# Kernel optimization log

Hardware: AMD Instinct MI355X
Metric: run time of the kernel (lower is better)

Reference implementation:

```python
import jax, jax.numpy as jnp
import numpy as np

DIM = 256
HALF = DIM // 2
B, S = 32, 4096
U_MAX = 4096          # upper bound on number of unique tree positions (positions < S)
MAX_DEPTH = 13        # bitlen(S) covers all path lengths for positions <= S


def setup_inputs() -> dict:
    key = jax.random.key(0)
    k1, k2, k3, k4, k5 = jax.random.split(key, 5)
    token_types = jax.random.randint(k1, (B, S), 0, 5, dtype=jnp.int32)
    node_positions = jax.random.randint(k2, (B, S), 0, S, dtype=jnp.int32)
    small_vals = jax.random.randint(k3, (B, S), 0, 4, dtype=jnp.int32)
    # deBruijn tokens (type 4) reference tree positions -> values must lie in unique(node_positions)
    token_values = jnp.where(token_types == 4, node_positions,
                   jnp.where(token_types == 3, -1, small_vals)).astype(jnp.int32)
    primitives = jax.random.normal(k4, (2, HALF, HALF), dtype=jnp.float32)
    identity = jnp.ones((1, HALF), dtype=jnp.float32)
    embed_weight = jax.random.normal(k5, (11, HALF), dtype=jnp.float32)
    return {"token_types": token_types, "token_values": token_values,
            "node_positions": node_positions, "primitives": primitives,
            "identity": identity, "embed_weight": embed_weight}


def cayley(X):
    # torch orthogonal(..., orthogonal_map='cayley'): A = tril(X) - tril(X)^T (skew), Q = (I - A/2)^{-1}(I + A/2)
    A = jnp.tril(X)
    A = A - jnp.swapaxes(A, -1, -2)
    I = jnp.eye(X.shape[-1], dtype=X.dtype)
    return jnp.linalg.solve(I - 0.5 * A, I + 0.5 * A)


def _forward(token_types, token_values, node_positions, primitives, identity, embed_weight):
    Q = cayley(primitives)                                   # [2, h, h] orthogonal maps
    flat_pos = node_positions.ravel()
    uniq, inv = jnp.unique(flat_pos, return_inverse=True, size=U_MAX, fill_value=S)
    inv = inv.ravel()

    # binary path of pos: bit d of pos for d < bitlen(pos)-1, padded with 2 (pos<=1 -> empty path)
    d = jnp.arange(MAX_DEPTH, dtype=uniq.dtype)
    bits = (uniq[:, None] >> d) & 1                           # [U, D]
    valid = (uniq[:, None] >> (d + 1)) > 0
    word = jnp.where(valid, bits, 2)                          # [U, D]

    maps0 = jnp.broadcast_to(identity, (U_MAX, HALF)).astype(primitives.dtype)

    def step(maps, b):                                        # maps [U, h], b [U]
        m0 = maps @ Q[0].T                                    # linear(maps, primitives[0])
        m1 = maps @ Q[1].T
        maps = jnp.where((b == 0)[:, None], m0,
                jnp.where((b == 1)[:, None], m1, maps))
        return maps, None

    path_emb, _ = jax.lax.scan(step, maps0, word.T)           # [U, h]

    pos_enc = path_emb[inv].reshape(B, S, HALF)               # positional encodings

    sos = token_types == 0
    bop = token_types == 1
    nop = token_types == 2
    oos = (token_types == 3) & (token_values == -1)
    db = token_types == 4

    emb_idx = jnp.where(bop, token_values + 1,
              jnp.where(nop, token_values + 5, 0))
    type_emb = embed_weight[emb_idx]                          # [B, S, h]

    db_idx = jnp.searchsorted(uniq, jnp.clip(token_values, 0, S - 1))  # bucketize into unique positions
    db_emb = path_emb[db_idx]                                 # [B, S, h]

    content = jnp.zeros_like(pos_enc)
    content = jnp.where(sos[..., None], embed_weight[0], content)
    content = jnp.where((bop | nop)[..., None], type_emb, content)
    content = jnp.where(db[..., None], db_emb, content)
    content = jnp.where(oos[..., None], embed_weight[10], content)

    return jnp.concatenate([content, pos_enc], axis=-1)       # [B, S, DIM]


def reference(token_types, token_values, node_positions, primitives, identity, embed_weight):
    return _forward(token_types, token_values, node_positions, primitives, identity, embed_weight)
```

## Files before the change

### kernel.cpp

```cpp
#include <hip/hip_runtime.h>

#define HALF 128
#define NMAT 16384
#define NTOK 131072

typedef float f4 __attribute__((ext_vector_type(4)));

__global__ __launch_bounds__(512) void cayley_qt(const float* __restrict__ prim,
                                                 float* __restrict__ QT) {
    __shared__ __align__(16) float Xs[128 * 129];
    __shared__ __align__(16) float CpT[2][16][132];
    __shared__ __align__(16) float Rp [2][16][128];
    __shared__ __align__(16) float Dcol[2][16][20];

    const int b = blockIdx.x;
    const float* __restrict__ X = prim + b * NMAT;
    const int t  = threadIdx.x;
    const int c  = t & 127;
    const int q  = t >> 7;
    const int r0 = q << 5;

    for (int idx4 = t; idx4 < 4096; idx4 += 512) {
        int gi = idx4 << 2;
        float4 v = *(const float4*)(X + gi);
        int r = gi >> 7, cc = gi & 127;
        float* p = &Xs[r * 129 + cc];
        p[0] = v.x; p[1] = v.y; p[2] = v.z; p[3] = v.w;
    }
    __syncthreads();

    float reg[32];
    #pragma unroll
    for (int i = 0; i < 32; ++i) {
        int r  = r0 + i;
        int mx = r > c ? r : c;
        int mn = r ^ c ^ mx;
        float x = Xs[mx * 129 + mn];
        reg[i] = (r == c) ? 1.0f : (r > c ? 0.5f * x : -0.5f * x);
    }

    #pragma unroll
    for (int s = 0; s < 8; ++s) {
        const int  p     = s & 1;
        const int  k0    = s << 4;
        const int  q0    = s >> 1;
        const int  kl    = (s & 1) << 4;
        const bool panel = (c >= k0) && (c < k0 + 16);

        if (panel) {
            const int m = c - k0;
            #pragma unroll
            for (int i = 0; i < 32; i += 4)
                *(float4*)&CpT[p][m][r0 + i] =
                    make_float4(reg[i], reg[i+1], reg[i+2], reg[i+3]);
        }
        if (q == q0) {
            #pragma unroll
            for (int j = 0; j < 16; ++j) Rp[p][j][c] = reg[kl + j];
        }
        __syncthreads();

        if (t < 64) {
            const int cp = t & 15, q4 = t >> 4;
            float dd[4];
            #pragma unroll
            for (int i = 0; i < 4; ++i) dd[i] = Rp[p][q4 * 4 + i][k0 + cp];
            #pragma unroll
            for (int k = 0; k < 16; ++k) {
                float cv[4];
                #pragma unroll
                for (int i = 0; i < 4; ++i) cv[i] = __shfl(dd[i], (q4 << 4) | k);
                float rv   = __shfl(dd[k & 3], ((k >> 2) << 4) | cp);
                float dkk  = __shfl(rv, k);
                float dinv = 1.0f / dkk;
                float sv   = rv * dinv;
                bool  own  = (cp == k);
                float rf   = own ? dinv : sv;
                #pragma unroll
                for (int i = 0; i < 4; ++i)
                    dd[i] = own ? (-dd[i] * dinv) : fmaf(-cv[i], sv, dd[i]);
                dd[k & 3] = (q4 == (k >> 2)) ? rf : dd[k & 3];
            }
            #pragma unroll
            for (int i = 0; i < 4; ++i) Dcol[p][cp][q4 * 4 + i] = dd[i];
        }
        __syncthreads();

        float coeff[16];
        if (!panel) {
            #pragma unroll
            for (int j = 0; j < 16; ++j) coeff[j] = 0.0f;
            #pragma unroll
            for (int j = 0; j < 16; ++j) {
                float rpj = Rp[p][j][c];
                #pragma unroll
                for (int mq = 0; mq < 16; mq += 4) {
                    float4 dv = *(const float4*)&Dcol[p][j][mq];
                    coeff[mq+0] = fmaf(dv.x, rpj, coeff[mq+0]);
                    coeff[mq+1] = fmaf(dv.y, rpj, coeff[mq+1]);
                    coeff[mq+2] = fmaf(dv.z, rpj, coeff[mq+2]);
                    coeff[mq+3] = fmaf(dv.w, rpj, coeff[mq+3]);
                }
            }
        } else {
            const int mp = c - k0;
            #pragma unroll
            for (int j = 0; j < 16; ++j) coeff[j] = Dcol[p][mp][j];
            #pragma unroll
            for (int i = 0; i < 32; ++i) reg[i] = 0.0f;
        }

        #pragma unroll
        for (int m = 0; m < 16; ++m) {
            float cm = coeff[m];
            #pragma unroll
            for (int i = 0; i < 32; i += 4) {
                float4 c4 = *(const float4*)&CpT[p][m][r0 + i];
                reg[i+0] = fmaf(-c4.x, cm, reg[i+0]);
                reg[i+1] = fmaf(-c4.y, cm, reg[i+1]);
                reg[i+2] = fmaf(-c4.z, cm, reg[i+2]);
                reg[i+3] = fmaf(-c4.w, cm, reg[i+3]);
            }
        }
        if (q == q0) {
            #pragma unroll
            for (int j = 0; j < 16; ++j) reg[kl + j] = coeff[j];
        }
    }

    float* __restrict__ out = QT + b * NMAT;
    #pragma unroll
    for (int i = 0; i < 32; ++i) {
        int r = r0 + i;
        out[r * HALF + c] = 2.0f * reg[i] - (r == c ? 1.0f : 0.0f);
    }
}

__global__ __launch_bounds__(256) void path_base(const float* __restrict__ QT,
                                                 const float* __restrict__ ident,
                                                 float* __restrict__ P) {
    __shared__ __align__(16) float vs[2][4][HALF];
    const int t    = threadIdx.x;
    const int rg   = t >> 6;
    const int jj   = (t & 63) << 1;
    const int v    = (blockIdx.x << 2) + rg;
    const int vmax = (blockIdx.x << 2) + 3;

    float2 cv = *(const float2*)&ident[jj];
    *(float2*)&vs[0][rg][jj] = cv;
    __syncthreads();

    int cur = 0;
    for (int d = 0; d < 8; ++d) {
        if ((vmax >> (d + 1)) == 0) break;
        const bool valid = (v >> (d + 1)) > 0;
        const float* __restrict__ Qm = QT + (((v >> d) & 1) ? NMAT : 0);
        float2 acc = make_float2(0.f, 0.f);
        #pragma unroll 4
        for (int cc = 0; cc < 128; cc += 4) {
            float4 v4 = *(const float4*)&vs[cur][rg][cc];
            float2 q0 = *(const float2*)&Qm[(cc+0)*HALF + jj];
            float2 q1 = *(const float2*)&Qm[(cc+1)*HALF + jj];
            float2 q2 = *(const float2*)&Qm[(cc+2)*HALF + jj];
            float2 q3 = *(const float2*)&Qm[(cc+3)*HALF + jj];
            acc.x = fmaf(v4.x,q0.x, fmaf(v4.y,q1.x, fmaf(v4.z,q2.x, fmaf(v4.w,q3.x, acc.x))));
            acc.y = fmaf(v4.x,q0.y, fmaf(v4.y,q1.y, fmaf(v4.z,q2.y, fmaf(v4.w,q3.y, acc.y))));
        }
        if (valid) cv = acc;
        *(float2*)&vs[cur ^ 1][rg][jj] = cv;
        __syncthreads();
        cur ^= 1;
    }
    *(float2*)&P[v * HALF + jj] = cv;
}

__global__ __launch_bounds__(256) void path_upper(const float* __restrict__ QT,
                                                  float* __restrict__ P) {
    __shared__ __align__(16) float vs[2][8][HALF];
    const int t  = threadIdx.x;
    const int j  = t & 127;
    const int h  = t >> 7;
    const int k  = 2 + (blockIdx.x >> 4);
    const int r0 = (blockIdx.x & 15) << 3;

    float acc[4];
    #pragma unroll
    for (int rr = 0; rr < 4; ++rr)
        acc[rr] = P[(128 + r0 + h * 4 + rr) * HALF + j];

    int p = 0;
    for (int d = 7; d < 13; ++d) {
        if ((k >> (d - 6)) == 0) break;
        const float* __restrict__ Qm = QT + (((k >> (d - 7)) & 1) ? NMAT : 0);
        #pragma unroll
        for (int rr = 0; rr < 4; ++rr) vs[p][h * 4 + rr][j] = acc[rr];
        __syncthreads();

        float nacc[4] = {0.f, 0.f, 0.f, 0.f};
        #pragma unroll 4
        for (int cc = 0; cc < 128; cc += 4) {
            float q0 = Qm[(cc + 0) * HALF + j];
            float q1 = Qm[(cc + 1) * HALF + j];
            float q2 = Qm[(cc + 2) * HALF + j];
            float q3 = Qm[(cc + 3) * HALF + j];
            #pragma unroll
            for (int rr = 0; rr < 4; ++rr) {
                float4 v4 = *(const float4*)&vs[p][h * 4 + rr][cc];
                nacc[rr] = fmaf(v4.x, q0,
                           fmaf(v4.y, q1,
                           fmaf(v4.z, q2,
                           fmaf(v4.w, q3, nacc[rr]))));
            }
        }
        #pragma unroll
        for (int rr = 0; rr < 4; ++rr) acc[rr] = nacc[rr];
        p ^= 1;
    }

    #pragma unroll
    for (int rr = 0; rr < 4; ++rr)
        P[((k << 7) | (r0 + h * 4 + rr)) * HALF + j] = acc[rr];
}

__global__ __launch_bounds__(256) void emit_out(const int* __restrict__ tt,
                                                const int* __restrict__ tv,
                                                const int* __restrict__ np,
                                                const float* __restrict__ P,
                                                const float* __restrict__ emb,
                                                float* __restrict__ out) {
    const int i  = (blockIdx.x << 2) + (threadIdx.x >> 6);
    const int jj = (threadIdx.x & 63) << 2;
    const int ty = tt[i];
    const int v  = tv[i];
    f4 val;
    if (jj < 128) {
        if (ty == 0)      val = *(const f4*)&emb[jj];
        else if (ty == 1) val = *(const f4*)&emb[(v + 1) * HALF + jj];
        else if (ty == 2) val = *(const f4*)&emb[(v + 5) * HALF + jj];
        else if (ty == 4) {
            int vc = v < 0 ? 0 : (v > 4095 ? 4095 : v);
            val = *(const f4*)&P[vc * HALF + jj];
        } else if (v == -1) val = *(const f4*)&emb[10 * HALF + jj];
        else { f4 z = {0.f, 0.f, 0.f, 0.f}; val = z; }
    } else {
        const int p = np[i];
        val = *(const f4*)&P[p * HALF + (jj - 128)];
    }
    __builtin_nontemporal_store(val, (f4*)&out[i * 256 + jj]);
}

extern "C" void kernel_launch(void* const* d_in, const int* in_sizes, int n_in,
                              void* d_out, int out_size, void* d_ws, size_t ws_size,
                              hipStream_t stream) {
    const int*   token_types = (const int*)  d_in[0];
    const int*   token_vals  = (const int*)  d_in[1];
    const int*   node_pos    = (const int*)  d_in[2];
    const float* prim        = (const float*)d_in[3];
    const float* ident       = (const float*)d_in[4];
    const float* emb         = (const float*)d_in[5];
    float* out = (float*)d_out;

    float* QT = (float*)d_ws;
    float* P  = (float*)((char*)d_ws + 262144);

    cayley_qt  <<<2,   512, 0, stream>>>(prim, QT);
    path_base  <<<64,  256, 0, stream>>>(QT, ident, P);
    path_upper <<<480, 256, 0, stream>>>(QT, P);
    emit_out   <<<NTOK / 4, 256, 0, stream>>>(token_types, token_vals, node_pos,
                                              P, emb, out);
}
```

Measured before the change: 275.7 us.

## Retile Cayley solve to 4x8 register blocks with precomputed panel update in shared memory

Each thread in the Cayley matrix inversion kernel now holds a 4x8 sub-block instead of a 32-row column strip. Each panel step precomputes the update matrix RB = D*R cooperatively in shared memory, rather than every thread computing its own 16 coefficients redundantly. The rank-16 update then reads row-panel coefficients and RB rows as float4 vectors, and the final stores are vectorized. This cuts redundant FLOPs and improves shared-memory reuse, at the cost of one extra __syncthreads per panel step.

```diff
diff --git a/kernel.cpp b/kernel.cpp
--- a/kernel.cpp
+++ b/kernel.cpp
@@ -9,54 +9,66 @@
 __global__ __launch_bounds__(512) void cayley_qt(const float* __restrict__ prim,
                                                  float* __restrict__ QT) {
     __shared__ __align__(16) float Xs[128 * 129];
-    __shared__ __align__(16) float CpT[2][16][132];
-    __shared__ __align__(16) float Rp [2][16][128];
-    __shared__ __align__(16) float Dcol[2][16][20];
+    __shared__ __align__(16) float Cp[2][128][20];
+    __shared__ __align__(16) float Rp[16][132];
+    __shared__ __align__(16) float Dcol[16][20];
+    __shared__ __align__(16) float RB[16][132];
 
     const int b = blockIdx.x;
     const float* __restrict__ X = prim + b * NMAT;
     const int t  = threadIdx.x;
-    const int c  = t & 127;
-    const int q  = t >> 7;
-    const int r0 = q << 5;
+    const int rg = t >> 4;
+    const int cg = t & 15;
 
     for (int idx4 = t; idx4 < 4096; idx4 += 512) {
         int gi = idx4 << 2;
         float4 v = *(const float4*)(X + gi);
         int r = gi >> 7, cc = gi & 127;
-        float* p = &Xs[r * 129 + cc];
-        p[0] = v.x; p[1] = v.y; p[2] = v.z; p[3] = v.w;
+        float* xp = &Xs[r * 129 + cc];
+        xp[0] = v.x; xp[1] = v.y; xp[2] = v.z; xp[3] = v.w;
     }
     __syncthreads();
 
-    float reg[32];
-    #pragma unroll
-    for (int i = 0; i < 32; ++i) {
-        int r  = r0 + i;
-        int mx = r > c ? r : c;
-        int mn = r ^ c ^ mx;
-        float x = Xs[mx * 129 + mn];
-        reg[i] = (r == c) ? 1.0f : (r > c ? 0.5f * x : -0.5f * x);
+    float reg[4][8];
+    #pragma unroll
+    for (int i = 0; i < 4; ++i) {
+        const int r = (rg << 2) + i;
+        #pragma unroll
+        for (int jj = 0; jj < 8; ++jj) {
+            const int c = (cg << 3) + jj;
+            int mx = r > c ? r : c;
+            int mn = r ^ c ^ mx;
+            float x = Xs[mx * 129 + mn];
+            reg[i][jj] = (r == c) ? 1.0f : (r > c ? 0.5f * x : -0.5f * x);
+        }
     }
 
     #pragma unroll
     for (int s = 0; s < 8; ++s) {
-        const int  p     = s & 1;
-        const int  k0    = s << 4;
-        const int  q0    = s >> 1;
-        const int  kl    = (s & 1) << 4;
-        const bool panel = (c >= k0) && (c < k0 + 16);
-
-        if (panel) {
-            const int m = c - k0;
-            #pragma unroll
-            for (int i = 0; i < 32; i += 4)
-                *(float4*)&CpT[p][m][r0 + i] =
-                    make_float4(reg[i], reg[i+1], reg[i+2], reg[i+3]);
-        }
-        if (q == q0) {
-            #pragma unroll
-            for (int j = 0; j < 16; ++j) Rp[p][j][c] = reg[kl + j];
+        const int  p    = s & 1;
+        const int  k0   = s << 4;
+        const bool pubC = (cg >> 1) == s;
+        const bool pubR = (rg >> 2) == s;
+
+        if (pubC) {
+            const int mb = (cg & 1) << 3;
+            #pragma unroll
+            for (int i = 0; i < 4; ++i) {
+                *(float4*)&Cp[p][(rg << 2) + i][mb] =
+                    make_float4(reg[i][0], reg[i][1], reg[i][2], reg[i][3]);
+                *(float4*)&Cp[p][(rg << 2) + i][mb + 4] =
+                    make_float4(reg[i][4], reg[i][5], reg[i][6], reg[i][7]);
+            }
+        }
+        if (pubR) {
+            const int jb = (rg & 3) << 2;
+            #pragma unroll
+            for (int i = 0; i < 4; ++i) {
+                *(float4*)&Rp[jb + i][cg << 3] =
+                    make_float4(reg[i][0], reg[i][1], reg[i][2], reg[i][3]);
+                *(float4*)&Rp[jb + i][(cg << 3) + 4] =
+                    make_float4(reg[i][4], reg[i][5], reg[i][6], reg[i][7]);
+            }
         }
         __syncthreads();
 
@@ -64,7 +76,7 @@
             const int cp = t & 15, q4 = t >> 4;
             float dd[4];
             #pragma unroll
-            for (int i = 0; i < 4; ++i) dd[i] = Rp[p][q4 * 4 + i][k0 + cp];
+            for (int i = 0; i < 4; ++i) dd[i] = Rp[q4 * 4 + i][k0 + cp];
             #pragma unroll
             for (int k = 0; k < 16; ++k) {
                 float cv[4];
@@ -82,57 +94,96 @@
                 dd[k & 3] = (q4 == (k >> 2)) ? rf : dd[k & 3];
             }
             #pragma unroll
-            for (int i = 0; i < 4; ++i) Dcol[p][cp][q4 * 4 + i] = dd[i];
-        }
-        __syncthreads();
-
-        float coeff[16];
-        if (!panel) {
-            #pragma unroll
-            for (int j = 0; j < 16; ++j) coeff[j] = 0.0f;
-            #pragma unroll
-            for (int j = 0; j < 16; ++j) {
-                float rpj = Rp[p][j][c];
+            for (int i = 0; i < 4; ++i) Dcol[cp][q4 * 4 + i] = dd[i];
+        }
+        __syncthreads();
+
+        {
+            const int m  = t >> 5;
+            const int qd = t & 31;
+            const int cb = qd << 2;
+            float4 acc;
+            if ((qd >> 2) == s) {
+                acc.x = Dcol[cb + 0 - k0][m];
+                acc.y = Dcol[cb + 1 - k0][m];
+                acc.z = Dcol[cb + 2 - k0][m];
+                acc.w = Dcol[cb + 3 - k0][m];
+            } else {
+                acc = make_float4(0.f, 0.f, 0.f, 0.f);
                 #pragma unroll
-                for (int mq = 0; mq < 16; mq += 4) {
-                    float4 dv = *(const float4*)&Dcol[p][j][mq];
-                    coeff[mq+0] = fmaf(dv.x, rpj, coeff[mq+0]);
-                    coeff[mq+1] = fmaf(dv.y, rpj, coeff[mq+1]);
-                    coeff[mq+2] = fmaf(dv.z, rpj, coeff[mq+2]);
-                    coeff[mq+3] = fmaf(dv.w, rpj, coeff[mq+3]);
+                for (int j = 0; j < 16; ++j) {
+                    float  dj = Dcol[j][m];
+                    float4 r4 = *(const float4*)&Rp[j][cb];
+                    acc.x = fmaf(dj, r4.x, acc.x);
+                    acc.y = fmaf(dj, r4.y, acc.y);
+                    acc.z = fmaf(dj, r4.z, acc.z);
+                    acc.w = fmaf(dj, r4.w, acc.w);
                 }
             }
-        } else {
-            const int mp = c - k0;
-            #pragma unroll
-            for (int j = 0; j < 16; ++j) coeff[j] = Dcol[p][mp][j];
-            #pragma unroll
-            for (int i = 0; i < 32; ++i) reg[i] = 0.0f;
-        }
-
+            *(float4*)&RB[m][cb] = acc;
+        }
+        __syncthreads();
+
+        float crs[4][16];
+        #pragma unroll
+        for (int i = 0; i < 4; ++i)
+            #pragma unroll
+            for (int mq = 0; mq < 4; ++mq) {
+                float4 v = *(const float4*)&Cp[p][(rg << 2) + i][mq << 2];
+                crs[i][4 * mq + 0] = v.x; crs[i][4 * mq + 1] = v.y;
+                crs[i][4 * mq + 2] = v.z; crs[i][4 * mq + 3] = v.w;
+            }
+        if (pubC) {
+            #pragma unroll
+            for (int i = 0; i < 4; ++i)
+                #pragma unroll
+                for (int jj = 0; jj < 8; ++jj) reg[i][jj] = 0.0f;
+        }
         #pragma unroll
         for (int m = 0; m < 16; ++m) {
-            float cm = coeff[m];
-            #pragma unroll
-            for (int i = 0; i < 32; i += 4) {
-                float4 c4 = *(const float4*)&CpT[p][m][r0 + i];
-                reg[i+0] = fmaf(-c4.x, cm, reg[i+0]);
-                reg[i+1] = fmaf(-c4.y, cm, reg[i+1]);
-                reg[i+2] = fmaf(-c4.z, cm, reg[i+2]);
-                reg[i+3] = fmaf(-c4.w, cm, reg[i+3]);
-            }
-        }
-        if (q == q0) {
-            #pragma unroll
-            for (int j = 0; j < 16; ++j) reg[kl + j] = coeff[j];
+            float4 rb0 = *(const float4*)&RB[m][cg << 3];
+            float4 rb1 = *(const float4*)&RB[m][(cg << 3) + 4];
+            #pragma unroll
+            for (int i = 0; i < 4; ++i) {
+                float cm = crs[i][m];
+                reg[i][0] = fmaf(-cm, rb0.x, reg[i][0]);
+                reg[i][1] = fmaf(-cm, rb0.y, reg[i][1]);
+                reg[i][2] = fmaf(-cm, rb0.z, reg[i][2]);
+                reg[i][3] = fmaf(-cm, rb0.w, reg[i][3]);
+                reg[i][4] = fmaf(-cm, rb1.x, reg[i][4]);
+                reg[i][5] = fmaf(-cm, rb1.y, reg[i][5]);
+                reg[i][6] = fmaf(-cm, rb1.z, reg[i][6]);
+                reg[i][7] = fmaf(-cm, rb1.w, reg[i][7]);
+            }
+        }
+        if (pubR) {
+            const int jb = (rg & 3) << 2;
+            #pragma unroll
+            for (int i = 0; i < 4; ++i) {
+                float4 a = *(const float4*)&RB[jb + i][cg << 3];
+                float4 b2 = *(const float4*)&RB[jb + i][(cg << 3) + 4];
+                reg[i][0] = a.x;  reg[i][1] = a.y;  reg[i][2] = a.z;  reg[i][3] = a.w;
+                reg[i][4] = b2.x; reg[i][5] = b2.y; reg[i][6] = b2.z; reg[i][7] = b2.w;
+            }
         }
     }
 
     float* __restrict__ out = QT + b * NMAT;
     #pragma unroll
-    for (int i = 0; i < 32; ++i) {
-        int r = r0 + i;
-        out[r * HALF + c] = 2.0f * reg[i] - (r == c ? 1.0f : 0.0f);
+    for (int i = 0; i < 4; ++i) {
+        const int r  = (rg << 2) + i;
+        const int c0 = cg << 3;
+        float4 o0, o1;
+        o0.x = 2.0f * reg[i][0] - (r == c0 + 0 ? 1.0f : 0.0f);
+        o0.y = 2.0f * reg[i][1] - (r == c0 + 1 ? 1.0f : 0.0f);
+        o0.z = 2.0f * reg[i][2] - (r == c0 + 2 ? 1.0f : 0.0f);
+        o0.w = 2.0f * reg[i][3] - (r == c0 + 3 ? 1.0f : 0.0f);
+        o1.x = 2.0f * reg[i][4] - (r == c0 + 4 ? 1.0f : 0.0f);
+        o1.y = 2.0f * reg[i][5] - (r == c0 + 5 ? 1.0f : 0.0f);
+        o1.z = 2.0f * reg[i][6] - (r == c0 + 6 ? 1.0f : 0.0f);
+        o1.w = 2.0f * reg[i][7] - (r == c0 + 7 ? 1.0f : 0.0f);
+        *(float4*)&out[r * HALF + c0]     = o0;
+        *(float4*)&out[r * HALF + c0 + 4] = o1;
     }
 }
 
```

New measurement: 405.2 us (median of 3 runs). 1.47x slower.

## Split Cayley solve into per-panel kernels to spread the update across blocks

Applied to the files above, without the earlier changes.

The single 2-block Cayley Gauss-Jordan kernel is replaced by 16 launches that alternate a panel kernel (2 blocks, which inverts the 16x16 pivot block and forms the scaled pivot rows) with an update kernel (16 blocks, which updates 16-row slices). The aim is to use more CUs for the matrix update instead of leaving two blocks to do all the work. In exchange it adds 14 extra kernel launches with global-memory round trips through the workspace. The per-step work is small, so launch overhead may dominate.

```diff
diff --git a/kernel.cpp b/kernel.cpp
--- a/kernel.cpp
+++ b/kernel.cpp
@@ -6,134 +6,156 @@
 
 typedef float f4 __attribute__((ext_vector_type(4)));
 
-__global__ __launch_bounds__(512) void cayley_qt(const float* __restrict__ prim,
-                                                 float* __restrict__ QT) {
-    __shared__ __align__(16) float Xs[128 * 129];
-    __shared__ __align__(16) float CpT[2][16][132];
-    __shared__ __align__(16) float Rp [2][16][128];
-    __shared__ __align__(16) float Dcol[2][16][20];
-
-    const int b = blockIdx.x;
-    const float* __restrict__ X = prim + b * NMAT;
+__device__ __forceinline__ float nval(const float* __restrict__ X, int r, int c) {
+    int mx = r > c ? r : c;
+    int mn = r ^ c ^ mx;
+    float x = X[mx * HALF + mn];
+    return (r == c) ? 1.0f : (r > c ? 0.5f * x : -0.5f * x);
+}
+
+
+template<int S, bool FIRST>
+__global__ __launch_bounds__(256) void k1_panel(const float* __restrict__ prim,
+                                                const float* __restrict__ W,
+                                                float* __restrict__ RBws) {
+    __shared__ __align__(16) float Rs[16][132];
+    __shared__ float Dc[16][17];
+    const int b  = blockIdx.x;
     const int t  = threadIdx.x;
-    const int c  = t & 127;
-    const int q  = t >> 7;
-    const int r0 = q << 5;
-
-    for (int idx4 = t; idx4 < 4096; idx4 += 512) {
-        int gi = idx4 << 2;
-        float4 v = *(const float4*)(X + gi);
-        int r = gi >> 7, cc = gi & 127;
-        float* p = &Xs[r * 129 + cc];
-        p[0] = v.x; p[1] = v.y; p[2] = v.z; p[3] = v.w;
+    const int k0 = S << 4;
+    const float* __restrict__ X  = prim + b * NMAT;
+    const float* __restrict__ Wb = W + b * NMAT;
+
+    {
+        const int j  = t >> 4;
+        const int c0 = (t & 15) << 3;
+        if (FIRST) {
+            #pragma unroll
+            for (int u = 0; u < 8; ++u) Rs[j][c0 + u] = nval(X, k0 + j, c0 + u);
+        } else {
+            float4 a  = *(const float4*)&Wb[(k0 + j) * HALF + c0];
+            float4 b2 = *(const float4*)&Wb[(k0 + j) * HALF + c0 + 4];
+            *(float4*)&Rs[j][c0]     = a;
+            *(float4*)&Rs[j][c0 + 4] = b2;
+        }
     }
     __syncthreads();
 
-    float reg[32];
-    #pragma unroll
-    for (int i = 0; i < 32; ++i) {
-        int r  = r0 + i;
-        int mx = r > c ? r : c;
-        int mn = r ^ c ^ mx;
-        float x = Xs[mx * 129 + mn];
-        reg[i] = (r == c) ? 1.0f : (r > c ? 0.5f * x : -0.5f * x);
-    }
-
-    #pragma unroll
-    for (int s = 0; s < 8; ++s) {
-        const int  p     = s & 1;
-        const int  k0    = s << 4;
-        const int  q0    = s >> 1;
-        const int  kl    = (s & 1) << 4;
-        const bool panel = (c >= k0) && (c < k0 + 16);
-
-        if (panel) {
-            const int m = c - k0;
-            #pragma unroll
-            for (int i = 0; i < 32; i += 4)
-                *(float4*)&CpT[p][m][r0 + i] =
-                    make_float4(reg[i], reg[i+1], reg[i+2], reg[i+3]);
-        }
-        if (q == q0) {
-            #pragma unroll
-            for (int j = 0; j < 16; ++j) Rp[p][j][c] = reg[kl + j];
-        }
-        __syncthreads();
-
-        if (t < 64) {
-            const int cp = t & 15, q4 = t >> 4;
-            float dd[4];
-            #pragma unroll
-            for (int i = 0; i < 4; ++i) dd[i] = Rp[p][q4 * 4 + i][k0 + cp];
-            #pragma unroll
-            for (int k = 0; k < 16; ++k) {
-                float cv[4];
+    if (t < 64) {
+        const int cp = t & 15, q4 = t >> 4;
+        float dd[4];
+        #pragma unroll
+        for (int i = 0; i < 4; ++i) dd[i] = Rs[q4 * 4 + i][k0 + cp];
+        #pragma unroll
+        for (int k = 0; k < 16; ++k) {
+            float cv[4];
+            #pragma unroll
+            for (int i = 0; i < 4; ++i) cv[i] = __shfl(dd[i], (q4 << 4) | k);
+            float rv   = __shfl(dd[k & 3], ((k >> 2) << 4) | cp);
+            float dkk  = __shfl(rv, k);
+            float dinv = 1.0f / dkk;
+            float sv   = rv * dinv;
+            bool  own  = (cp == k);
+            float rf   = own ? dinv : sv;
+            #pragma unroll
+            for (int i = 0; i < 4; ++i)
+                dd[i] = own ? (-dd[i] * dinv) : fmaf(-cv[i], sv, dd[i]);
+            dd[k & 3] = (q4 == (k >> 2)) ? rf : dd[k & 3];
+        }
+        #pragma unroll
+        for (int i = 0; i < 4; ++i) Dc[cp][q4 * 4 + i] = dd[i];
+    }
+    __syncthreads();
+
+    {
+        const int m  = t >> 4;
+        const int c0 = (t & 15) << 3;
+        float* __restrict__ RBb = RBws + b * (16 * HALF);
+        if (c0 == k0 || c0 == k0 + 8) {
+            #pragma unroll
+            for (int u = 0; u < 8; ++u) RBb[m * HALF + c0 + u] = Dc[c0 + u - k0][m];
+        } else {
+            float acc[8] = {0.f,0.f,0.f,0.f,0.f,0.f,0.f,0.f};
+            #pragma unroll
+            for (int j = 0; j < 16; ++j) {
+                float dj = Dc[j][m];
                 #pragma unroll
-                for (int i = 0; i < 4; ++i) cv[i] = __shfl(dd[i], (q4 << 4) | k);
-                float rv   = __shfl(dd[k & 3], ((k >> 2) << 4) | cp);
-                float dkk  = __shfl(rv, k);
-                float dinv = 1.0f / dkk;
-                float sv   = rv * dinv;
-                bool  own  = (cp == k);
-                float rf   = own ? dinv : sv;
-                #pragma unroll
-                for (int i = 0; i < 4; ++i)
-                    dd[i] = own ? (-dd[i] * dinv) : fmaf(-cv[i], sv, dd[i]);
-                dd[k & 3] = (q4 == (k >> 2)) ? rf : dd[k & 3];
+                for (int u = 0; u < 8; ++u)
+                    acc[u] = fmaf(dj, Rs[j][c0 + u], acc[u]);
             }
-            #pragma unroll
-            for (int i = 0; i < 4; ++i) Dcol[p][cp][q4 * 4 + i] = dd[i];
-        }
-        __syncthreads();
-
-        float coeff[16];
-        if (!panel) {
-            #pragma unroll
-            for (int j = 0; j < 16; ++j) coeff[j] = 0.0f;
-            #pragma unroll
-            for (int j = 0; j < 16; ++j) {
-                float rpj = Rp[p][j][c];
-                #pragma unroll
-                for (int mq = 0; mq < 16; mq += 4) {
-                    float4 dv = *(const float4*)&Dcol[p][j][mq];
-                    coeff[mq+0] = fmaf(dv.x, rpj, coeff[mq+0]);
-                    coeff[mq+1] = fmaf(dv.y, rpj, coeff[mq+1]);
-                    coeff[mq+2] = fmaf(dv.z, rpj, coeff[mq+2]);
-                    coeff[mq+3] = fmaf(dv.w, rpj, coeff[mq+3]);
-                }
-            }
+            *(float4*)&RBb[m * HALF + c0]     = make_float4(acc[0], acc[1], acc[2], acc[3]);
+            *(float4*)&RBb[m * HALF + c0 + 4] = make_float4(acc[4], acc[5], acc[6], acc[7]);
+        }
+    }
+}
+
+template<int S, bool FIRST, bool LAST>
+__global__ __launch_bounds__(256) void k1_update(const float* __restrict__ prim,
+                                                 float* __restrict__ W,
+                                                 const float* __restrict__ RBws) {
+    __shared__ __align__(16) float RBs[16][132];
+    __shared__ float Cs[16][17];
+    const int blk = blockIdx.x;
+    const int b   = blk >> 3;
+    const int rg  = blk & 7;
+    const int r0  = rg << 4;
+    const int t   = threadIdx.x;
+    const int k0  = S << 4;
+    const float* __restrict__ X   = prim + b * NMAT;
+    float* __restrict__ Wb        = W + b * NMAT;
+    const float* __restrict__ RBb = RBws + b * (16 * HALF);
+
+    {
+        const int m  = t >> 4;
+        const int c0 = (t & 15) << 3;
+        *(float4*)&RBs[m][c0]     = *(const float4*)&RBb[m * HALF + c0];
+        *(float4*)&RBs[m][c0 + 4] = *(const float4*)&RBb[m * HALF + c0 + 4];
+    }
+    {
+        const int rr = t >> 4, m = t & 15;
+        Cs[rr][m] = FIRST ? nval(X, r0 + rr, k0 + m)
+                          : Wb[(r0 + rr) * HALF + k0 + m];
+    }
+    __syncthreads();
+
+    const int rr = t >> 4;
+    const int r  = r0 + rr;
+    const int c0 = (t & 15) << 3;
+    float w[8];
+
+    if (rg == S) {
+        #pragma unroll
+        for (int u = 0; u < 8; ++u) w[u] = RBs[rr][c0 + u];
+    } else {
+        const bool pan = (c0 == k0) || (c0 == k0 + 8);
+        if (pan) {
+            #pragma unroll
+            for (int u = 0; u < 8; ++u) w[u] = 0.0f;
+        } else if (FIRST) {
+            #pragma unroll
+            for (int u = 0; u < 8; ++u) w[u] = nval(X, r, c0 + u);
         } else {
-            const int mp = c - k0;
-            #pragma unroll
-            for (int j = 0; j < 16; ++j) coeff[j] = Dcol[p][mp][j];
-            #pragma unroll
-            for (int i = 0; i < 32; ++i) reg[i] = 0.0f;
-        }
-
+            float4 a  = *(const float4*)&Wb[r * HALF + c0];
+            float4 b2 = *(const float4*)&Wb[r * HALF + c0 + 4];
+            w[0]=a.x; w[1]=a.y; w[2]=a.z; w[3]=a.w;
+            w[4]=b2.x; w[5]=b2.y; w[6]=b2.z; w[7]=b2.w;
+        }
         #pragma unroll
         for (int m = 0; m < 16; ++m) {
-            float cm = coeff[m];
-            #pragma unroll
-            for (int i = 0; i < 32; i += 4) {
-                float4 c4 = *(const float4*)&CpT[p][m][r0 + i];
-                reg[i+0] = fmaf(-c4.x, cm, reg[i+0]);
-                reg[i+1] = fmaf(-c4.y, cm, reg[i+1]);
-                reg[i+2] = fmaf(-c4.z, cm, reg[i+2]);
-                reg[i+3] = fmaf(-c4.w, cm, reg[i+3]);
-            }
-        }
-        if (q == q0) {
-            #pragma unroll
-            for (int j = 0; j < 16; ++j) reg[kl + j] = coeff[j];
-        }
-    }
-
-    float* __restrict__ out = QT + b * NMAT;
-    #pragma unroll
-    for (int i = 0; i < 32; ++i) {
-        int r = r0 + i;
-        out[r * HALF + c] = 2.0f * reg[i] - (r == c ? 1.0f : 0.0f);
-    }
+            float cm = Cs[rr][m];
+            #pragma unroll
+            for (int u = 0; u < 8; ++u)
+                w[u] = fmaf(-cm, RBs[m][c0 + u], w[u]);
+        }
+    }
+
+    if (LAST) {
+        #pragma unroll
+        for (int u = 0; u < 8; ++u)
+            w[u] = 2.0f * w[u] - ((r == c0 + u) ? 1.0f : 0.0f);
+    }
+    *(float4*)&Wb[r * HALF + c0]     = make_float4(w[0], w[1], w[2], w[3]);
+    *(float4*)&Wb[r * HALF + c0 + 4] = make_float4(w[4], w[5], w[6], w[7]);
 }
 
 __global__ __launch_bounds__(256) void path_base(const float* __restrict__ QT,
@@ -262,8 +284,25 @@
 
     float* QT = (float*)d_ws;
     float* P  = (float*)((char*)d_ws + 262144);
-
-    cayley_qt  <<<2,   512, 0, stream>>>(prim, QT);
+    float* RB = (float*)((char*)d_ws + 2359296);
+
+    k1_panel <0, true        ><<<2,  256, 0, stream>>>(prim, QT, RB);
+    k1_update<0, true,  false><<<16, 256, 0, stream>>>(prim, QT, RB);
+    k1_panel <1, false       ><<<2,  256, 0, stream>>>(prim, QT, RB);
+    k1_update<1, false, false><<<16, 256, 0, stream>>>(prim, QT, RB);
+    k1_panel <2, false       ><<<2,  256, 0, stream>>>(prim, QT, RB);
+    k1_update<2, false, false><<<16, 256, 0, stream>>>(prim, QT, RB);
+    k1_panel <3, false       ><<<2,  256, 0, stream>>>(prim, QT, RB);
+    k1_update<3, false, false><<<16, 256, 0, stream>>>(prim, QT, RB);
+    k1_panel <4, false       ><<<2,  256, 0, stream>>>(prim, QT, RB);
+    k1_update<4, false, false><<<16, 256, 0, stream>>>(prim, QT, RB);
+    k1_panel <5, false       ><<<2,  256, 0, stream>>>(prim, QT, RB);
+    k1_update<5, false, false><<<16, 256, 0, stream>>>(prim, QT, RB);
+    k1_panel <6, false       ><<<2,  256, 0, stream>>>(prim, QT, RB);
+    k1_update<6, false, false><<<16, 256, 0, stream>>>(prim, QT, RB);
+    k1_panel <7, false       ><<<2,  256, 0, stream>>>(prim, QT, RB);
+    k1_update<7, false, true ><<<16, 256, 0, stream>>>(prim, QT, RB);
+
     path_base  <<<64,  256, 0, stream>>>(QT, ident, P);
     path_upper <<<480, 256, 0, stream>>>(QT, P);
     emit_out   <<<NTOK / 4, 256, 0, stream>>>(token_types, token_vals, node_pos,
```

Measured after the change: 304.7 us. 1.11x slower.
